# Kernel tuning notes

Hardware: AMD Instinct MI355X
Metric: run time of the kernel (lower is better)

Reference implementation:

```python
import jax, jax.numpy as jnp
import numpy as np

B, T, DIM, H, DH = 4, 2048, 1024, 16, 64
NEG = -1.0e9


def setup_inputs() -> dict:
    key = jax.random.key(0)
    ks = jax.random.split(key, 12)
    inner = H * DH
    s_in = 1.0 / np.sqrt(DIM)
    s_out = 1.0 / np.sqrt(inner)
    q = jax.random.normal(ks[0], (B, T, DIM), jnp.float32)
    k = jax.random.normal(ks[1], (B, T, DIM), jnp.float32)
    v = jax.random.normal(ks[2], (B, T, DIM), jnp.float32)
    # nn.Linear weights stored as [out, in]; we keep [in, out] for x @ W
    W_q = jax.random.uniform(ks[3], (DIM, inner), jnp.float32, -s_in, s_in)
    b_q = jax.random.uniform(ks[4], (inner,), jnp.float32, -s_in, s_in)
    W_k = jax.random.uniform(ks[5], (DIM, inner), jnp.float32, -s_in, s_in)
    b_k = jax.random.uniform(ks[6], (inner,), jnp.float32, -s_in, s_in)
    W_v = jax.random.uniform(ks[7], (DIM, inner), jnp.float32, -s_in, s_in)
    b_v = jax.random.uniform(ks[8], (inner,), jnp.float32, -s_in, s_in)
    W_o = jax.random.uniform(ks[9], (inner, DIM), jnp.float32, -s_out, s_out)
    b_o = jax.random.uniform(ks[10], (DIM,), jnp.float32, -s_out, s_out)
    # causal mask: True = masked (strict upper triangle), broadcastable [1,1,T,T]
    causal_mask = jnp.triu(jnp.ones((T, T), bool), k=1)[None, None]
    # context mask: True = keep; random padding pattern with col 0 always valid
    context_mask = jax.random.bernoulli(ks[11], 0.9, (B, T)).at[:, 0].set(True)
    return {"q": q, "k": k, "v": v,
            "W_q": W_q, "b_q": b_q, "W_k": W_k, "b_k": b_k,
            "W_v": W_v, "b_v": b_v, "W_o": W_o, "b_o": b_o,
            "causal_mask": causal_mask, "context_mask": context_mask}


def reference(q, k, v, W_q, b_q, W_k, b_k, W_v, b_v, W_o, b_o,
              causal_mask, context_mask):
    scale = DH ** -0.5
    split = lambda x: x.reshape(x.shape[0], x.shape[1], H, DH).transpose(0, 2, 1, 3)
    qh = split(q @ W_q + b_q)  # [b,h,t,d]
    kh = split(k @ W_k + b_k)
    vh = split(v @ W_v + b_v)
    scores = jnp.einsum('bhid,bhjd->bhij', qh * scale, kh)
    scores = jnp.where(context_mask[:, None, None, :], scores, NEG)
    scores = jnp.where(causal_mask, NEG, scores)
    probs = jax.nn.softmax(scores, axis=-1)
    out = jnp.einsum('bhij,bhjd->bhid', probs, vh)
    out = out.transpose(0, 2, 1, 3).reshape(B, T, H * DH)
    return out @ W_o + b_o
```

## Files before the change

kernel.cpp:

```cpp
#include <hip/hip_runtime.h>
#include <hip/hip_bf16.h>
#include <cstdint>
#include <cstddef>

#define DEV static __device__ __forceinline__

typedef __attribute__((ext_vector_type(8))) short short8;
typedef __attribute__((ext_vector_type(4))) short short4v;
typedef __attribute__((ext_vector_type(4))) float floatx4;

#define BB 4
#define TT 2048
#define DIMM 1024
#define HH 16
#define DHH 64
#define MM (BB*TT)
#define QBLK 128
#define NQT (TT/QBLK)
#define M0F 12.0f

DEV unsigned short f2bu(float f) {
    unsigned int u = __float_as_uint(f);
    unsigned int r = (u + 0x7fffu + ((u >> 16) & 1u)) >> 16;
    return (unsigned short)r;
}

DEV unsigned long long pack4(float a, float b, float c, float d) {
    return (unsigned long long)f2bu(a) | ((unsigned long long)f2bu(b) << 16) |
           ((unsigned long long)f2bu(c) << 32) | ((unsigned long long)f2bu(d) << 48);
}

DEV unsigned int pk2(float lo, float hi) {
    __hip_bfloat162 h = __float22bfloat162_rn(make_float2(lo, hi));
    unsigned int r;
    __builtin_memcpy(&r, &h, 4);
    return r;
}

DEV unsigned long long pk4(float a, float b, float c, float d) {
    return (unsigned long long)pk2(a, b) | ((unsigned long long)pk2(c, d) << 32);
}

DEV void gload16(const void* g, void* l) {
    __builtin_amdgcn_global_load_lds(
        (const __attribute__((address_space(1))) unsigned int*)g,
        (__attribute__((address_space(3))) unsigned int*)l, 16, 0, 0);
}

#define MFMA16(a, b, c) __builtin_amdgcn_mfma_f32_16x16x32_bf16((a), (b), (c), 0, 0, 0)

#if defined(__has_builtin)
#if __has_builtin(__builtin_amdgcn_mfma_f32_16x16x16bf16_1k)
#define HAVE_MFMA_K16 1
#endif
#endif

DEV floatx4 mfma_k16(short4v a, short4v b, floatx4 c) {
#ifdef HAVE_MFMA_K16
    return __builtin_amdgcn_mfma_f32_16x16x16bf16_1k(a, b, c, 0, 0, 0);
#else
    asm volatile("v_mfma_f32_16x16x16_bf16 %0, %1, %2, %0" : "+v"(c) : "v"(a), "v"(b));
    return c;
#endif
}

__global__ __launch_bounds__(256) void ctx_bias(const unsigned char* __restrict__ raw,
                                                float* __restrict__ out) {
    __shared__ int nz1, nz23;
    if (threadIdx.x == 0) { nz1 = 0; nz23 = 0; }
    __syncthreads();
    int a1 = 0, a23 = 0;
    for (int i = threadIdx.x; i < BB * TT; i += 256) {
        unsigned char vb = raw[i];
        int m = i & 3;
        if (vb) { if (m == 1) a1 = 1; else if (m >= 2) a23 = 1; }
    }
    if (a1) atomicOr(&nz1, 1);
    if (a23) atomicOr(&nz23, 1);
    __syncthreads();
    const int mode = nz1 ? 2 : (nz23 ? 1 : 0);
    for (int i = threadIdx.x; i < BB * TT; i += 256) {
        bool keep;
        if (mode == 2)      keep = raw[i] != 0;
        else if (mode == 0) keep = raw[(size_t)4 * i] != 0;
        else                keep = (raw[(size_t)4 * i + 2] | raw[(size_t)4 * i + 3]) != 0;
        out[i] = keep ? -M0F : -3.0e38f;
    }
}

__global__ __launch_bounds__(256) void wtrans(const float* __restrict__ W0, const float* __restrict__ W1,
                                              const float* __restrict__ W2, const float* __restrict__ W3,
                                              unsigned short* __restrict__ out) {
    const float* W = blockIdx.y == 0 ? W0 : blockIdx.y == 1 ? W1 : blockIdx.y == 2 ? W2 : W3;
    unsigned short* O = out + (size_t)blockIdx.y * DIMM * DIMM;
    const int tx = blockIdx.x & 15, ty = blockIdx.x >> 4;
    __shared__ float s[64][65];
    const int tid = threadIdx.x;
#pragma unroll
    for (int j = 0; j < 4; ++j) {
        int c = tid + 256 * j;
        int r = c >> 4, c4 = c & 15;
        float4 vv = *reinterpret_cast<const float4*>(&W[(size_t)(ty * 64 + r) * DIMM + tx * 64 + c4 * 4]);
        s[r][c4 * 4 + 0] = vv.x; s[r][c4 * 4 + 1] = vv.y;
        s[r][c4 * 4 + 2] = vv.z; s[r][c4 * 4 + 3] = vv.w;
    }
    __syncthreads();
#pragma unroll
    for (int j = 0; j < 4; ++j) {
        int c = tid + 256 * j;
        int n = c >> 4, k4 = c & 15;
        unsigned long long pk = pack4(s[k4 * 4 + 0][n], s[k4 * 4 + 1][n], s[k4 * 4 + 2][n], s[k4 * 4 + 3][n]);
        *reinterpret_cast<unsigned long long*>(&O[(size_t)(tx * 64 + n) * DIMM + ty * 64 + k4 * 4]) = pk;
    }
}

__global__ __launch_bounds__(256) void cvt_bf16(const float* __restrict__ in,
                                                unsigned short* __restrict__ out) {
    const size_t i = ((size_t)blockIdx.x * 256 + threadIdx.x) * 8;
    float4 a = *reinterpret_cast<const float4*>(&in[i]);
    float4 b = *reinterpret_cast<const float4*>(&in[i + 4]);
    unsigned long long lo = pk4(a.x, a.y, a.z, a.w);
    unsigned long long hi = pk4(b.x, b.y, b.z, b.w);
    ulonglong2 v; v.x = lo; v.y = hi;
    *reinterpret_cast<ulonglong2*>(&out[i]) = v;
}

template <int OMODE>
__global__ __launch_bounds__(256) void gemm_bf16(const unsigned short* __restrict__ Ab,
                                                 const unsigned short* __restrict__ Bt,
                                                 const float* __restrict__ bias,
                                                 void* __restrict__ Cp, float scale) {
    __shared__ unsigned short As[2][128 * 64];
    __shared__ unsigned short Bs[2][128 * 64];
    const int tid = threadIdx.x, lane = tid & 63, g = lane >> 4, lq = lane & 15;
    const int wid = tid >> 6;
    const int mbase = blockIdx.x * 128, nbase = blockIdx.y * 128;
    const int wm = (wid >> 1) * 64, wn = (wid & 1) * 64;
    floatx4 acc[4][4];
#pragma unroll
    for (int i = 0; i < 4; ++i)
#pragma unroll
        for (int j = 0; j < 4; ++j) acc[i][j] = (floatx4){0.f, 0.f, 0.f, 0.f};

#define STAGE(buf, k0)                                                              \
    {                                                                               \
        _Pragma("unroll")                                                           \
        for (int j = 0; j < 4; ++j) {                                               \
            const int c = j * 256 + tid;                                            \
            const int row = c >> 3, ci = c & 7;                                     \
            const int sc = ci ^ (row & 7);                                          \
            gload16(&Ab[(size_t)(mbase + row) * DIMM + (k0) + sc * 8], &As[buf][c * 8]); \
            gload16(&Bt[(size_t)(nbase + row) * DIMM + (k0) + sc * 8], &Bs[buf][c * 8]); \
        }                                                                           \
    }

    STAGE(0, 0);
    asm volatile("s_waitcnt vmcnt(0)");
    __syncthreads();
    int cur = 0;
    for (int k0 = 0; k0 < DIMM; k0 += 64) {
        if (k0 + 64 < DIMM) STAGE(cur ^ 1, k0 + 64);
#pragma unroll
        for (int kk = 0; kk < 2; ++kk) {
            short8 af[4], bf[4];
#pragma unroll
            for (int i = 0; i < 4; ++i) {
                const int ra = wm + i * 16 + lq;
                af[i] = *reinterpret_cast<const short8*>(&As[cur][ra * 64 + ((kk * 4 + g) ^ (ra & 7)) * 8]);
                const int rb = wn + i * 16 + lq;
                bf[i] = *reinterpret_cast<const short8*>(&Bs[cur][rb * 64 + ((kk * 4 + g) ^ (rb & 7)) * 8]);
            }
#pragma unroll
            for (int i = 0; i < 4; ++i)
#pragma unroll
                for (int j2 = 0; j2 < 4; ++j2)
                    acc[i][j2] = MFMA16(af[i], bf[j2], acc[i][j2]);
        }
        __syncthreads();
        cur ^= 1;
    }
#undef STAGE

#pragma unroll
    for (int i = 0; i < 4; ++i) {
#pragma unroll
        for (int j = 0; j < 4; ++j) {
            const int col = nbase + wn + j * 16 + lq;
            const float bvv = bias[col];
            const int row0 = mbase + wm + i * 16 + g * 4;
            if (OMODE == 2) {
                float* C = (float*)Cp;
#pragma unroll
                for (int r = 0; r < 4; ++r)
                    C[(size_t)(row0 + r) * DIMM + col] = acc[i][j][r] + bvv;
            } else if (OMODE == 0) {
                unsigned short* C = (unsigned short*)Cp;
#pragma unroll
                for (int r = 0; r < 4; ++r)
                    C[(size_t)(row0 + r) * DIMM + col] = f2bu((acc[i][j][r] + bvv) * scale);
            } else {
                unsigned short* C = (unsigned short*)Cp;
                const int b = row0 >> 11, t0 = row0 & (TT - 1);
                const int h = col >> 6, d = col & 63;
                unsigned long long pk = pk4(acc[i][j][0] + bvv, acc[i][j][1] + bvv,
                                            acc[i][j][2] + bvv, acc[i][j][3] + bvv);
                *reinterpret_cast<unsigned long long*>(
                    &C[((size_t)(b * HH + h) * DHH + d) * TT + t0]) = pk;
            }
        }
    }
}

__global__ __launch_bounds__(512, 4) void attn128(const unsigned short* __restrict__ Q,
                                                  const unsigned short* __restrict__ Km,
                                                  const unsigned short* __restrict__ Vt,
                                                  const float* __restrict__ ctxb,
                                                  unsigned short* __restrict__ O) {
    const int pair = blockIdx.x >> 6, h = blockIdx.x & 15, b = (blockIdx.x >> 4) & 3;
    const int tid = threadIdx.x, lane = tid & 63, g = lane >> 4, lq = lane & 15, wid = tid >> 6;

    __shared__ unsigned short Qs[QBLK * 64];
    __shared__ unsigned short Ks[2][64 * 64];
    __shared__ unsigned short Vs[2][64 * 64];
    __shared__ float sbias[TT];

    const unsigned short* Vbase = Vt + (size_t)(b * HH + h) * DHH * TT;
    const int srow = tid >> 3, sdc = tid & 7;
    const int soff = (srow * 128 + sdc * 16) ^ ((srow & 7) << 4);
    const short4v vone = {(short)0x3F80, (short)0x3F80, (short)0x3F80, (short)0x3F80};

    *reinterpret_cast<float4*>(&sbias[tid * 4]) =
        *reinterpret_cast<const float4*>(&ctxb[b * TT + tid * 4]);

    for (int part = 0; part < 2; ++part) {
        const int qt = (part == 0) ? pair : (NQT - 1 - pair);
        const int qbase = qt * QBLK;
        const size_t rowQ = (size_t)(b * TT + qbase);
        const int nkv = 2 * qt + 2;

        __syncthreads();
#pragma unroll
        for (int j = 0; j < 2; ++j) {
            int ci = j * 512 + tid;
            int row = ci >> 3, dc = ci & 7;
            *reinterpret_cast<float4*>((char*)Qs + ((row * 128 + dc * 16) ^ ((row & 7) << 4))) =
                *reinterpret_cast<const float4*>(&Q[(rowQ + row) * DIMM + h * DHH + dc * 8]);
        }
        {
            float4 k0v = *reinterpret_cast<const float4*>(&Km[(size_t)(b * TT + srow) * DIMM + h * DHH + sdc * 8]);
            float4 v0v = *reinterpret_cast<const float4*>(&Vbase[(size_t)srow * TT + sdc * 8]);
            *reinterpret_cast<float4*>((char*)Ks[0] + soff) = k0v;
            *reinterpret_cast<float4*>((char*)Vs[0] + soff) = v0v;
        }
        __syncthreads();

        short8 qf0, qf1;
        {
            const int r = wid * 16 + lq;
            const int sw = (r & 7) << 4;
            qf0 = *reinterpret_cast<const short8*>((char*)Qs + ((r * 128 + g * 16) ^ sw));
            qf1 = *reinterpret_cast<const short8*>((char*)Qs + ((r * 128 + 64 + g * 16) ^ sw));
        }

        floatx4 oacc[4];
#pragma unroll
        for (int f = 0; f < 4; ++f) oacc[f] = (floatx4){0.f, 0.f, 0.f, 0.f};
        floatx4 lacc = (floatx4){0.f, 0.f, 0.f, 0.f};
        const int qwave_min = qbase + wid * 16;
        const int qg = qwave_min + lq;

        for (int kt = 0; kt < nkv; ++kt) {
            const int cur = kt & 1;
            const int kvb = kt * 64;
            const bool pf = (kt + 1 < nkv);
            float4 kreg, vreg;
            if (pf) {
                const int kvn = kvb + 64;
                kreg = *reinterpret_cast<const float4*>(&Km[(size_t)(b * TT + kvn + srow) * DIMM + h * DHH + sdc * 8]);
                vreg = *reinterpret_cast<const float4*>(&Vbase[(size_t)srow * TT + kvn + sdc * 8]);
            }
            if (kvb <= qwave_min + 15) {
                const bool needC = (kvb + 63 > qwave_min);
                float p[4][4];
                __builtin_amdgcn_s_setprio(1);
#pragma unroll
                for (int f = 0; f < 4; ++f) {
                    const int r = f * 16 + lq;
                    const int sw = (r & 7) << 4;
                    short8 kf0 = *reinterpret_cast<const short8*>((char*)Ks[cur] + ((r * 128 + g * 16) ^ sw));
                    short8 kf1 = *reinterpret_cast<const short8*>((char*)Ks[cur] + ((r * 128 + 64 + g * 16) ^ sw));
                    const float4 bias = *reinterpret_cast<const float4*>(&sbias[kvb + f * 16 + g * 4]);
                    floatx4 t = (floatx4){bias.x, bias.y, bias.z, bias.w};
                    t = MFMA16(kf0, qf0, t);
                    t = MFMA16(kf1, qf1, t);
#pragma unroll
                    for (int r2 = 0; r2 < 4; ++r2) {
                        float sv = t[r2];
                        if (needC) {
                            const int kv = kvb + f * 16 + g * 4 + r2;
                            if (kv > qg) sv = -3.0e38f;
                        }
                        p[f][r2] = exp2f(sv);
                    }
                }
                __builtin_amdgcn_s_setprio(0);
                short4v w[4];
#pragma unroll
                for (int f = 0; f < 4; ++f) {
                    unsigned long long pw = pk4(p[f][0], p[f][1], p[f][2], p[f][3]);
                    __builtin_memcpy(&w[f], &pw, 8);
                }
                __builtin_amdgcn_s_setprio(1);
#pragma unroll
                for (int f = 0; f < 4; ++f) {
                    const int r = f * 16 + lq;
                    const int sw = (r & 7) << 4;
                    const int rb = r * 128;
#pragma unroll
                    for (int j = 0; j < 4; ++j) {
                        short4v av = *reinterpret_cast<const short4v*>(
                            (char*)Vs[cur] + ((rb + j * 32 + g * 8) ^ sw));
                        oacc[f] = mfma_k16(av, w[j], oacc[f]);
                    }
                }
#pragma unroll
                for (int j = 0; j < 4; ++j) lacc = mfma_k16(vone, w[j], lacc);
                __builtin_amdgcn_s_setprio(0);
#ifndef HAVE_MFMA_K16
                asm volatile("s_nop 7\ns_nop 7");
#endif
            }
            if (pf) {
                *reinterpret_cast<float4*>((char*)Ks[cur ^ 1] + soff) = kreg;
                *reinterpret_cast<float4*>((char*)Vs[cur ^ 1] + soff) = vreg;
            }
            __syncthreads();
        }

        const float inv = 1.f / lacc[0];
#pragma unroll
        for (int f = 0; f < 4; ++f) {
            unsigned long long pk = pk4(oacc[f][0] * inv, oacc[f][1] * inv,
                                        oacc[f][2] * inv, oacc[f][3] * inv);
            *reinterpret_cast<unsigned long long*>(
                &O[(rowQ + wid * 16 + lq) * DIMM + h * DHH + f * 16 + g * 4]) = pk;
        }
    }
}

extern "C" void kernel_launch(void* const* d_in, const int* in_sizes, int n_in,
                              void* d_out, int out_size, void* d_ws, size_t ws_size,
                              hipStream_t stream) {
    const float* q  = (const float*)d_in[0];
    const float* k  = (const float*)d_in[1];
    const float* v  = (const float*)d_in[2];
    const float* Wq = (const float*)d_in[3];
    const float* bq = (const float*)d_in[4];
    const float* Wk = (const float*)d_in[5];
    const float* bk = (const float*)d_in[6];
    const float* Wv = (const float*)d_in[7];
    const float* bv = (const float*)d_in[8];
    const float* Wo = (const float*)d_in[9];
    const float* bo = (const float*)d_in[10];
    const unsigned char* cmask = (const unsigned char*)d_in[12];

    unsigned short* Qp  = (unsigned short*)d_ws;
    unsigned short* Kp  = Qp + (size_t)MM * DIMM;
    unsigned short* Vtp = Kp + (size_t)MM * DIMM;
    unsigned short* AO  = Vtp + (size_t)MM * DIMM;
    unsigned short* Wt  = AO + (size_t)MM * DIMM;
    float* ctxb = (float*)(Wt + (size_t)4 * DIMM * DIMM);

    ctx_bias<<<dim3(1), dim3(256), 0, stream>>>(cmask, ctxb);
    wtrans<<<dim3(256, 4), dim3(256), 0, stream>>>(Wq, Wk, Wv, Wo, Wt);

    const float scale_q = 0.125f * 1.4426950408889634f;

    cvt_bf16<<<dim3(4096), dim3(256), 0, stream>>>(q, AO);
    gemm_bf16<0><<<dim3(64, 8), dim3(256), 0, stream>>>(AO, Wt,                           bq, Qp,  scale_q);
    cvt_bf16<<<dim3(4096), dim3(256), 0, stream>>>(k, AO);
    gemm_bf16<0><<<dim3(64, 8), dim3(256), 0, stream>>>(AO, Wt + (size_t)DIMM * DIMM,     bk, Kp,  1.f);
    cvt_bf16<<<dim3(4096), dim3(256), 0, stream>>>(v, AO);
    gemm_bf16<1><<<dim3(64, 8), dim3(256), 0, stream>>>(AO, Wt + (size_t)2 * DIMM * DIMM, bv, Vtp, 1.f);

    attn128<<<dim3(BB * HH * 8), dim3(512), 0, stream>>>(Qp, Kp, Vtp, ctxb, AO);

    gemm_bf16<2><<<dim3(64, 8), dim3(256), 0, stream>>>(AO, Wt + (size_t)3 * DIMM * DIMM, bo, d_out, 1.f);
}
```

Baseline: 215.4 us.

## Batch Q/K/V conversion and projection into single launches, use native exp2

The three separate bf16 conversion kernels and three projection GEMMs become one cvt3 launch and one proj3 launch, each indexed by grid z/y. This fills the GPU with 1536 GEMM blocks instead of 512 per launch and removes launch gaps. The bf16 copies of k and v are staged in the output buffer as scratch before the final GEMM overwrites it. Attention softmax also switches to the raw hardware exp2 builtin, trading exactness of exp2f for fewer instructions.

```diff
diff --git a/kernel.cpp b/kernel.cpp
--- a/kernel.cpp
+++ b/kernel.cpp
@@ -40,6 +40,15 @@
 DEV unsigned long long pk4(float a, float b, float c, float d) {
     return (unsigned long long)pk2(a, b) | ((unsigned long long)pk2(c, d) << 32);
 }
+
+#if defined(__has_builtin)
+#if __has_builtin(__builtin_amdgcn_exp2f)
+#define EXP2R(x) __builtin_amdgcn_exp2f(x)
+#endif
+#endif
+#ifndef EXP2R
+#define EXP2R(x) exp2f(x)
+#endif
 
 DEV void gload16(const void* g, void* l) {
     __builtin_amdgcn_global_load_lds(
@@ -114,22 +123,36 @@
     }
 }
 
-__global__ __launch_bounds__(256) void cvt_bf16(const float* __restrict__ in,
-                                                unsigned short* __restrict__ out) {
+__global__ __launch_bounds__(256) void cvt3(const float* __restrict__ q, const float* __restrict__ k,
+                                            const float* __restrict__ v,
+                                            unsigned short* __restrict__ oq, unsigned short* __restrict__ ok,
+                                            unsigned short* __restrict__ ov) {
+    const int z = blockIdx.y;
+    const float* in = z == 0 ? q : z == 1 ? k : v;
+    unsigned short* out = z == 0 ? oq : z == 1 ? ok : ov;
     const size_t i = ((size_t)blockIdx.x * 256 + threadIdx.x) * 8;
     float4 a = *reinterpret_cast<const float4*>(&in[i]);
     float4 b = *reinterpret_cast<const float4*>(&in[i + 4]);
     unsigned long long lo = pk4(a.x, a.y, a.z, a.w);
     unsigned long long hi = pk4(b.x, b.y, b.z, b.w);
-    ulonglong2 v; v.x = lo; v.y = hi;
-    *reinterpret_cast<ulonglong2*>(&out[i]) = v;
-}
-
-template <int OMODE>
-__global__ __launch_bounds__(256) void gemm_bf16(const unsigned short* __restrict__ Ab,
-                                                 const unsigned short* __restrict__ Bt,
-                                                 const float* __restrict__ bias,
-                                                 void* __restrict__ Cp, float scale) {
+    ulonglong2 w; w.x = lo; w.y = hi;
+    *reinterpret_cast<ulonglong2*>(&out[i]) = w;
+}
+
+__global__ __launch_bounds__(256) void proj3(const unsigned short* __restrict__ Aq,
+                                             const unsigned short* __restrict__ Ak,
+                                             const unsigned short* __restrict__ Av,
+                                             const unsigned short* __restrict__ Wt,
+                                             const float* __restrict__ bq, const float* __restrict__ bk,
+                                             const float* __restrict__ bv,
+                                             unsigned short* __restrict__ Qp, unsigned short* __restrict__ Kp,
+                                             unsigned short* __restrict__ Vtp, float scale_q) {
+    const int z = blockIdx.z;
+    const unsigned short* Ab = z == 0 ? Aq : z == 1 ? Ak : Av;
+    const unsigned short* Bt = Wt + (size_t)z * DIMM * DIMM;
+    const float* bias = z == 0 ? bq : z == 1 ? bk : bv;
+    const float scale = z == 0 ? scale_q : 1.f;
+
     __shared__ unsigned short As[2][128 * 64];
     __shared__ unsigned short Bs[2][128 * 64];
     const int tid = threadIdx.x, lane = tid & 63, g = lane >> 4, lq = lane & 15;
@@ -188,25 +211,88 @@
             const int col = nbase + wn + j * 16 + lq;
             const float bvv = bias[col];
             const int row0 = mbase + wm + i * 16 + g * 4;
-            if (OMODE == 2) {
-                float* C = (float*)Cp;
-#pragma unroll
-                for (int r = 0; r < 4; ++r)
-                    C[(size_t)(row0 + r) * DIMM + col] = acc[i][j][r] + bvv;
-            } else if (OMODE == 0) {
-                unsigned short* C = (unsigned short*)Cp;
+            if (z < 2) {
+                unsigned short* C = z == 0 ? Qp : Kp;
 #pragma unroll
                 for (int r = 0; r < 4; ++r)
                     C[(size_t)(row0 + r) * DIMM + col] = f2bu((acc[i][j][r] + bvv) * scale);
             } else {
-                unsigned short* C = (unsigned short*)Cp;
                 const int b = row0 >> 11, t0 = row0 & (TT - 1);
                 const int h = col >> 6, d = col & 63;
                 unsigned long long pk = pk4(acc[i][j][0] + bvv, acc[i][j][1] + bvv,
                                             acc[i][j][2] + bvv, acc[i][j][3] + bvv);
                 *reinterpret_cast<unsigned long long*>(
-                    &C[((size_t)(b * HH + h) * DHH + d) * TT + t0]) = pk;
-            }
+                    &Vtp[((size_t)(b * HH + h) * DHH + d) * TT + t0]) = pk;
+            }
+        }
+    }
+}
+
+__global__ __launch_bounds__(256) void gemm_out(const unsigned short* __restrict__ Ab,
+                                                const unsigned short* __restrict__ Bt,
+                                                const float* __restrict__ bias,
+                                                float* __restrict__ C) {
+    __shared__ unsigned short As[2][128 * 64];
+    __shared__ unsigned short Bs[2][128 * 64];
+    const int tid = threadIdx.x, lane = tid & 63, g = lane >> 4, lq = lane & 15;
+    const int wid = tid >> 6;
+    const int mbase = blockIdx.x * 128, nbase = blockIdx.y * 128;
+    const int wm = (wid >> 1) * 64, wn = (wid & 1) * 64;
+    floatx4 acc[4][4];
+#pragma unroll
+    for (int i = 0; i < 4; ++i)
+#pragma unroll
+        for (int j = 0; j < 4; ++j) acc[i][j] = (floatx4){0.f, 0.f, 0.f, 0.f};
+
+#define STAGE(buf, k0)                                                              \
+    {                                                                               \
+        _Pragma("unroll")                                                           \
+        for (int j = 0; j < 4; ++j) {                                               \
+            const int c = j * 256 + tid;                                            \
+            const int row = c >> 3, ci = c & 7;                                     \
+            const int sc = ci ^ (row & 7);                                          \
+            gload16(&Ab[(size_t)(mbase + row) * DIMM + (k0) + sc * 8], &As[buf][c * 8]); \
+            gload16(&Bt[(size_t)(nbase + row) * DIMM + (k0) + sc * 8], &Bs[buf][c * 8]); \
+        }                                                                           \
+    }
+
+    STAGE(0, 0);
+    asm volatile("s_waitcnt vmcnt(0)");
+    __syncthreads();
+    int cur = 0;
+    for (int k0 = 0; k0 < DIMM; k0 += 64) {
+        if (k0 + 64 < DIMM) STAGE(cur ^ 1, k0 + 64);
+#pragma unroll
+        for (int kk = 0; kk < 2; ++kk) {
+            short8 af[4], bf[4];
+#pragma unroll
+            for (int i = 0; i < 4; ++i) {
+                const int ra = wm + i * 16 + lq;
+                af[i] = *reinterpret_cast<const short8*>(&As[cur][ra * 64 + ((kk * 4 + g) ^ (ra & 7)) * 8]);
+                const int rb = wn + i * 16 + lq;
+                bf[i] = *reinterpret_cast<const short8*>(&Bs[cur][rb * 64 + ((kk * 4 + g) ^ (rb & 7)) * 8]);
+            }
+#pragma unroll
+            for (int i = 0; i < 4; ++i)
+#pragma unroll
+                for (int j2 = 0; j2 < 4; ++j2)
+                    acc[i][j2] = MFMA16(af[i], bf[j2], acc[i][j2]);
+        }
+        __syncthreads();
+        cur ^= 1;
+    }
+#undef STAGE
+
+#pragma unroll
+    for (int i = 0; i < 4; ++i) {
+#pragma unroll
+        for (int j = 0; j < 4; ++j) {
+            const int col = nbase + wn + j * 16 + lq;
+            const float bv = bias[col];
+            const int row0 = mbase + wm + i * 16 + g * 4;
+#pragma unroll
+            for (int r = 0; r < 4; ++r)
+                C[(size_t)(row0 + r) * DIMM + col] = acc[i][j][r] + bv;
         }
     }
 }
@@ -300,7 +386,7 @@
                             const int kv = kvb + f * 16 + g * 4 + r2;
                             if (kv > qg) sv = -3.0e38f;
                         }
-                        p[f][r2] = exp2f(sv);
+                        p[f][r2] = EXP2R(sv);
                     }
                 }
                 __builtin_amdgcn_s_setprio(0);
@@ -371,19 +457,18 @@
     unsigned short* Wt  = AO + (size_t)MM * DIMM;
     float* ctxb = (float*)(Wt + (size_t)4 * DIMM * DIMM);
 
+    unsigned short* dlo = (unsigned short*)d_out;
+    unsigned short* dhi = dlo + (size_t)MM * DIMM;
+
     ctx_bias<<<dim3(1), dim3(256), 0, stream>>>(cmask, ctxb);
     wtrans<<<dim3(256, 4), dim3(256), 0, stream>>>(Wq, Wk, Wv, Wo, Wt);
 
     const float scale_q = 0.125f * 1.4426950408889634f;
 
-    cvt_bf16<<<dim3(4096), dim3(256), 0, stream>>>(q, AO);
-    gemm_bf16<0><<<dim3(64, 8), dim3(256), 0, stream>>>(AO, Wt,                           bq, Qp,  scale_q);
-    cvt_bf16<<<dim3(4096), dim3(256), 0, stream>>>(k, AO);
-    gemm_bf16<0><<<dim3(64, 8), dim3(256), 0, stream>>>(AO, Wt + (size_t)DIMM * DIMM,     bk, Kp,  1.f);
-    cvt_bf16<<<dim3(4096), dim3(256), 0, stream>>>(v, AO);
-    gemm_bf16<1><<<dim3(64, 8), dim3(256), 0, stream>>>(AO, Wt + (size_t)2 * DIMM * DIMM, bv, Vtp, 1.f);
+    cvt3<<<dim3(4096, 3), dim3(256), 0, stream>>>(q, k, v, AO, dlo, dhi);
+    proj3<<<dim3(64, 8, 3), dim3(256), 0, stream>>>(AO, dlo, dhi, Wt, bq, bk, bv, Qp, Kp, Vtp, scale_q);
 
     attn128<<<dim3(BB * HH * 8), dim3(512), 0, stream>>>(Qp, Kp, Vtp, ctxb, AO);
 
-    gemm_bf16<2><<<dim3(64, 8), dim3(256), 0, stream>>>(AO, Wt + (size_t)3 * DIMM * DIMM, bo, d_out, 1.f);
-}
+    gemm_out<<<dim3(64, 8), dim3(256), 0, stream>>>(AO, Wt + (size_t)3 * DIMM * DIMM, bo, (float*)d_out);
+}
```

New measurement: 199.7 us, median of 3. 7.3% less time.
